# Kernel optimization log

Measured on AMD Instinct MI355X. Metric: run time of the kernel, lower is better.

## Reference

```python
import jax, jax.numpy as jnp
import numpy as np

H = 2048          # hidden_size
NH = 16           # num_attention_heads
HD = H // NH      # head_dim = 128
SCALE = 1.0 / np.sqrt(HD)


def setup_inputs() -> dict:
    key = jax.random.key(0)
    k1, k2, k3 = jax.random.split(key, 3)
    hidden_states = jax.random.normal(k1, (4, 2048, H), dtype=jnp.float32)
    # Linear weights stored as [in, out] (torch stores [out, in]; math y = x @ W + b)
    W_attn = jax.random.normal(k2, (H, 3 * H), dtype=jnp.float32) * 0.02
    b_attn = jnp.zeros((3 * H,), dtype=jnp.float32)
    W_proj = jax.random.normal(k3, (H, H), dtype=jnp.float32) * 0.02
    b_proj = jnp.zeros((H,), dtype=jnp.float32)
    return {"hidden_states": hidden_states, "W_attn": W_attn, "b_attn": b_attn,
            "W_proj": W_proj, "b_proj": b_proj}


def reference(hidden_states, W_attn, b_attn, W_proj, b_proj):
    B, S, _ = hidden_states.shape
    qkv = hidden_states @ W_attn + b_attn            # [B, S, 3H]
    q, k, v = jnp.split(qkv, 3, axis=-1)
    # split heads -> [B, NH, S, HD]
    def split_heads(t):
        return t.reshape(B, S, NH, HD).transpose(0, 2, 1, 3)
    q, k, v = split_heads(q), split_heads(k), split_heads(v)
    scores = jnp.einsum('bhqd,bhkd->bhqk', q, k) * SCALE   # [B, NH, S, S]
    causal = jnp.tril(jnp.ones((S, S), dtype=bool))
    scores = jnp.where(causal, scores, jnp.finfo(scores.dtype).min)
    attn = jax.nn.softmax(scores, axis=-1)
    out = jnp.einsum('bhqk,bhkd->bhqd', attn, v)           # [B, NH, S, HD]
    out = out.transpose(0, 2, 1, 3).reshape(B, S, H)       # merge heads
    out = out @ W_proj + b_proj
    return out
```

## Files before the change

kernel.cpp:

```cpp
#include <hip/hip_runtime.h>
#include <hip/hip_bf16.h>

typedef __bf16 bf16x8 __attribute__((ext_vector_type(8)));
typedef float  f32x4  __attribute__((ext_vector_type(4)));
typedef __hip_bfloat16 bf16;

#define MFMA16(a,b,c) __builtin_amdgcn_mfma_f32_16x16x32_bf16(a,b,c,0,0,0)

__device__ __forceinline__ void gload_lds16(const void* g, void* l){
  __builtin_amdgcn_global_load_lds((const __attribute__((address_space(1))) void*)g,
                                   (__attribute__((address_space(3))) void*)l, 16, 0, 0);
}

__global__ __launch_bounds__(256) void k_cvt(const float* __restrict__ in,
                                             bf16* __restrict__ out, int n4){
  int stride = gridDim.x * blockDim.x;
  for (int i = blockIdx.x * blockDim.x + threadIdx.x; i < n4; i += stride){
    float4 v = ((const float4*)in)[i];
    bf16 o[4] = {__float2bfloat16(v.x), __float2bfloat16(v.y),
                 __float2bfloat16(v.z), __float2bfloat16(v.w)};
    *(ushort4*)(out + 4*(size_t)i) = *(ushort4*)o;
  }
}

__global__ __launch_bounds__(256) void k_tr(const float* __restrict__ in,
                                            bf16* __restrict__ out, int R, int C){
  __shared__ float t[32][33];
  int c0 = blockIdx.x*32, r0 = blockIdx.y*32;
  int x = threadIdx.x, y0 = threadIdx.y;
  for (int j = y0; j < 32; j += 8) t[j][x] = in[(size_t)(r0+j)*C + c0 + x];
  __syncthreads();
  for (int j = y0; j < 32; j += 8)
    out[(size_t)(c0+j)*R + r0 + x] = __float2bfloat16(t[x][j]);
}

template<bool OUTF32>
__global__ __launch_bounds__(256,2) void k_gemm(const bf16* __restrict__ A,
                                                const bf16* __restrict__ Bt,
                                                const float* __restrict__ bias,
                                                void* __restrict__ Cv,
                                                int M, int N, int K){
  __shared__ bf16 As[128*32];
  __shared__ bf16 Bs[128*32];
  const int tid = threadIdx.x, w = tid>>6, l = tid&63;
  const int wm = w>>1, wn = w&1, lg = l>>4, li = l&15;
  const int m0 = blockIdx.y*128, n0 = blockIdx.x*128;

  f32x4 acc[4][4];
  #pragma unroll
  for (int m=0;m<4;m++)
    #pragma unroll
    for (int n=0;n<4;n++) acc[m][n] = (f32x4){0.f,0.f,0.f,0.f};

  for (int k0 = 0; k0 < K; k0 += 32){
    #pragma unroll
    for (int i=0;i<2;i++){
      int u = i*256 + w*64 + l;
      int r = u>>2, c = (u&3)*8;
      gload_lds16(A  + (size_t)(m0+r)*K + k0 + c, As + (size_t)(i*256 + w*64)*8);
      gload_lds16(Bt + (size_t)(n0+r)*K + k0 + c, Bs + (size_t)(i*256 + w*64)*8);
    }
    __syncthreads();
    bf16x8 af[4], bfv[4];
    #pragma unroll
    for (int m=0;m<4;m++) af[m]  = *(const bf16x8*)(As + (size_t)(wm*64 + m*16 + li)*32 + lg*8);
    #pragma unroll
    for (int n=0;n<4;n++) bfv[n] = *(const bf16x8*)(Bs + (size_t)(wn*64 + n*16 + li)*32 + lg*8);
    #pragma unroll
    for (int m=0;m<4;m++)
      #pragma unroll
      for (int n=0;n<4;n++)
        acc[m][n] = MFMA16(af[m], bfv[n], acc[m][n]);
    __syncthreads();
  }

  #pragma unroll
  for (int m=0;m<4;m++)
    #pragma unroll
    for (int n=0;n<4;n++)
      #pragma unroll
      for (int r4=0;r4<4;r4++){
        int row = m0 + wm*64 + m*16 + lg*4 + r4;
        int col = n0 + wn*64 + n*16 + li;
        float v = acc[m][n][r4] + bias[col];
        if (OUTF32) ((float*)Cv)[(size_t)row*N + col] = v;
        else        ((bf16*)Cv)[(size_t)row*N + col] = __float2bfloat16(v);
      }
}

#define ATT_SCALE 0.08838834764831845f

__global__ __launch_bounds__(256,2) void k_attn(const bf16* __restrict__ qkv,
                                                bf16* __restrict__ O){
  const int qb = blockIdx.x, h = blockIdx.y, b = blockIdx.z;
  const int tid = threadIdx.x, w = tid>>6, l = tid&63;
  const int lg = l>>4, li = l&15;
  const size_t RS = 6144;

  __shared__ bf16 Kt[64][136];
  __shared__ bf16 Vt[128][72];
  __shared__ bf16 Pt[4][32][72];

  const bf16* qptr = qkv + ((size_t)(b*2048 + qb*128 + w*32))*RS + h*128;
  bf16x8 qf[2][4];
  #pragma unroll
  for (int m=0;m<2;m++)
    #pragma unroll
    for (int ks=0;ks<4;ks++)
      qf[m][ks] = *(const bf16x8*)(qptr + (size_t)(m*16+li)*RS + ks*32 + lg*8);

  f32x4 acc[2][8];
  #pragma unroll
  for (int m=0;m<2;m++)
    #pragma unroll
    for (int n=0;n<8;n++) acc[m][n] = (f32x4){0.f,0.f,0.f,0.f};
  float mst[8], lst[8];
  #pragma unroll
  for (int i=0;i<8;i++){ mst[i] = -1e30f; lst[i] = 0.f; }

  const int nkt = 2*(qb+1);
  for (int kt = 0; kt < nkt; ++kt){
    const bf16* kbase = qkv + ((size_t)(b*2048 + kt*64))*RS + 2048 + h*128;
    #pragma unroll
    for (int i=0;i<4;i++){
      int u = i*256 + tid;
      int r = u>>4, c = (u&15)*8;
      *(bf16x8*)(&Kt[r][c]) = *(const bf16x8*)(kbase + (size_t)r*RS + c);
    }
    const bf16* vbase = qkv + ((size_t)(b*2048 + kt*64))*RS + 4096 + h*128;
    #pragma unroll
    for (int i=0;i<4;i++){
      int key = i*16 + (tid&15);
      int d0  = ((tid>>4)&15)*8;
      bf16x8 v = *(const bf16x8*)(vbase + (size_t)key*RS + d0);
      #pragma unroll
      for (int j=0;j<8;j++) Vt[d0+j][key] = ((const bf16*)&v)[j];
    }
    __syncthreads();

    f32x4 s[2][4];
    #pragma unroll
    for (int m=0;m<2;m++)
      #pragma unroll
      for (int n=0;n<4;n++) s[m][n] = (f32x4){0.f,0.f,0.f,0.f};
    #pragma unroll
    for (int ks=0;ks<4;ks++){
      bf16x8 kf[4];
      #pragma unroll
      for (int n=0;n<4;n++) kf[n] = *(const bf16x8*)(&Kt[n*16+li][ks*32 + lg*8]);
      #pragma unroll
      for (int m=0;m<2;m++)
        #pragma unroll
        for (int n=0;n<4;n++) s[m][n] = MFMA16(qf[m][ks], kf[n], s[m][n]);
    }

    #pragma unroll
    for (int m=0;m<2;m++)
      #pragma unroll
      for (int n=0;n<4;n++){
        int key = kt*64 + n*16 + li;
        #pragma unroll
        for (int r4=0;r4<4;r4++){
          int qrow = qb*128 + w*32 + m*16 + lg*4 + r4;
          float v = s[m][n][r4]*ATT_SCALE;
          s[m][n][r4] = (key <= qrow) ? v : -1e30f;
        }
      }

    #pragma unroll
    for (int m=0;m<2;m++)
      #pragma unroll
      for (int r4=0;r4<4;r4++){
        int idx = m*4 + r4;
        float rm = fmaxf(fmaxf(s[m][0][r4], s[m][1][r4]),
                         fmaxf(s[m][2][r4], s[m][3][r4]));
        rm = fmaxf(rm, __shfl_xor(rm, 1));
        rm = fmaxf(rm, __shfl_xor(rm, 2));
        rm = fmaxf(rm, __shfl_xor(rm, 4));
        rm = fmaxf(rm, __shfl_xor(rm, 8));
        float mnew = fmaxf(mst[idx], rm);
        float corr = __expf(mst[idx] - mnew);
        mst[idx] = mnew;
        float ps = 0.f;
        #pragma unroll
        for (int n=0;n<4;n++){
          float p = __expf(s[m][n][r4] - mnew);
          s[m][n][r4] = p; ps += p;
        }
        ps += __shfl_xor(ps, 1);
        ps += __shfl_xor(ps, 2);
        ps += __shfl_xor(ps, 4);
        ps += __shfl_xor(ps, 8);
        lst[idx] = lst[idx]*corr + ps;
        #pragma unroll
        for (int n=0;n<8;n++) acc[m][n][r4] *= corr;
      }

    #pragma unroll
    for (int m=0;m<2;m++)
      #pragma unroll
      for (int n=0;n<4;n++)
        #pragma unroll
        for (int r4=0;r4<4;r4++)
          Pt[w][m*16 + lg*4 + r4][n*16 + li] = __float2bfloat16(s[m][n][r4]);

    #pragma unroll
    for (int ks=0;ks<2;ks++){
      bf16x8 pa[2];
      #pragma unroll
      for (int m=0;m<2;m++) pa[m] = *(const bf16x8*)(&Pt[w][m*16+li][ks*32 + lg*8]);
      #pragma unroll
      for (int n=0;n<8;n++){
        bf16x8 vf = *(const bf16x8*)(&Vt[n*16+li][ks*32 + lg*8]);
        #pragma unroll
        for (int m=0;m<2;m++) acc[m][n] = MFMA16(pa[m], vf, acc[m][n]);
      }
    }
    __syncthreads();
  }

  bf16* obase = O + ((size_t)(b*2048 + qb*128 + w*32))*2048 + h*128;
  #pragma unroll
  for (int m=0;m<2;m++)
    #pragma unroll
    for (int n=0;n<8;n++)
      #pragma unroll
      for (int r4=0;r4<4;r4++){
        float v = acc[m][n][r4] / lst[m*4 + r4];
        obase[(size_t)(m*16 + lg*4 + r4)*2048 + n*16 + li] = __float2bfloat16(v);
      }
}

extern "C" void kernel_launch(void* const* d_in, const int* in_sizes, int n_in,
                              void* d_out, int out_size, void* d_ws, size_t ws_size,
                              hipStream_t stream) {
  const float* X      = (const float*)d_in[0];
  const float* W_attn = (const float*)d_in[1];
  const float* b_attn = (const float*)d_in[2];
  const float* W_proj = (const float*)d_in[3];
  const float* b_proj = (const float*)d_in[4];
  float* out = (float*)d_out;

  char* ws = (char*)d_ws;
  bf16* Xb  = (bf16*)(ws);
  bf16* Wat = (bf16*)(ws + 33554432);
  bf16* Wpt = (bf16*)(ws + 58720256);
  bf16* QKV = (bf16*)(ws + 67108864);
  bf16* Obf = Xb;

  k_cvt<<<2048, 256, 0, stream>>>(X, Xb, 8192*2048/4);
  k_tr <<<dim3(192,64), dim3(32,8), 0, stream>>>(W_attn, Wat, 2048, 6144);
  k_tr <<<dim3(64,64),  dim3(32,8), 0, stream>>>(W_proj, Wpt, 2048, 2048);

  k_gemm<false><<<dim3(48,64), 256, 0, stream>>>(Xb, Wat, b_attn, (void*)QKV, 8192, 6144, 2048);

  k_attn<<<dim3(16,16,4), 256, 0, stream>>>(QKV, Obf);

  k_gemm<true><<<dim3(16,64), 256, 0, stream>>>(Obf, Wpt, b_proj, (void*)out, 8192, 2048, 2048);
}
```

Baseline: 649.7 us.

## Swizzle attention LDS tiles, load K via direct-to-LDS, and reverse query block order

Replaces the padded LDS arrays for K, V and P in the attention kernel with unpadded byte buffers that use an XOR swizzle on 16-byte chunks to avoid bank conflicts. K tiles are now loaded with global_load_lds, which writes straight into LDS and skips the register round trip, and the global source address is permuted to match the swizzle. Query blocks are also launched in reverse so the longest causal blocks start first, which should improve load balance across the grid. The added risk is that the swizzle index math has to agree exactly between the global_load_lds writes, which are placed per wave and lane, and the reads.

```diff
diff --git a/kernel.cpp b/kernel.cpp
--- a/kernel.cpp
+++ b/kernel.cpp
@@ -11,6 +11,8 @@
   __builtin_amdgcn_global_load_lds((const __attribute__((address_space(1))) void*)g,
                                    (__attribute__((address_space(3))) void*)l, 16, 0, 0);
 }
+
+__device__ __forceinline__ int swzb(int row){ return ((row ^ (row>>3)) & 7) << 4; }
 
 __global__ __launch_bounds__(256) void k_cvt(const float* __restrict__ in,
                                              bf16* __restrict__ out, int n4){
@@ -92,14 +94,15 @@
 
 __global__ __launch_bounds__(256,2) void k_attn(const bf16* __restrict__ qkv,
                                                 bf16* __restrict__ O){
-  const int qb = blockIdx.x, h = blockIdx.y, b = blockIdx.z;
+  const int qb = 15 - blockIdx.x, h = blockIdx.y, b = blockIdx.z;
   const int tid = threadIdx.x, w = tid>>6, l = tid&63;
   const int lg = l>>4, li = l&15;
   const size_t RS = 6144;
-
-  __shared__ bf16 Kt[64][136];
-  __shared__ bf16 Vt[128][72];
-  __shared__ bf16 Pt[4][32][72];
+  const size_t RSB = RS*2;
+
+  __shared__ char Kt[64*256];
+  __shared__ char Vt[128*128];
+  __shared__ char Pt[4][32*128];
 
   const bf16* qptr = qkv + ((size_t)(b*2048 + qb*128 + w*32))*RS + h*128;
   bf16x8 qf[2][4];
@@ -120,12 +123,13 @@
 
   const int nkt = 2*(qb+1);
   for (int kt = 0; kt < nkt; ++kt){
-    const bf16* kbase = qkv + ((size_t)(b*2048 + kt*64))*RS + 2048 + h*128;
+    const char* kbase = (const char*)(qkv + ((size_t)(b*2048 + kt*64))*RS + 2048 + h*128);
     #pragma unroll
     for (int i=0;i<4;i++){
       int u = i*256 + tid;
-      int r = u>>4, c = (u&15)*8;
-      *(bf16x8*)(&Kt[r][c]) = *(const bf16x8*)(kbase + (size_t)r*RS + c);
+      int r = u>>4, cbl = (u&15)*16;
+      int cg = cbl ^ swzb(r);
+      gload_lds16(kbase + (size_t)r*RSB + cg, Kt + i*4096 + w*1024);
     }
     const bf16* vbase = qkv + ((size_t)(b*2048 + kt*64))*RS + 4096 + h*128;
     #pragma unroll
@@ -134,7 +138,8 @@
       int d0  = ((tid>>4)&15)*8;
       bf16x8 v = *(const bf16x8*)(vbase + (size_t)key*RS + d0);
       #pragma unroll
-      for (int j=0;j<8;j++) Vt[d0+j][key] = ((const bf16*)&v)[j];
+      for (int j=0;j<8;j++)
+        *(bf16*)(Vt + (d0+j)*128 + ((key*2) ^ swzb(d0+j))) = ((const bf16*)&v)[j];
     }
     __syncthreads();
 
@@ -147,7 +152,10 @@
     for (int ks=0;ks<4;ks++){
       bf16x8 kf[4];
       #pragma unroll
-      for (int n=0;n<4;n++) kf[n] = *(const bf16x8*)(&Kt[n*16+li][ks*32 + lg*8]);
+      for (int n=0;n<4;n++){
+        int row = n*16+li;
+        kf[n] = *(const bf16x8*)(Kt + row*256 + ((ks*64+lg*16) ^ swzb(row)));
+      }
       #pragma unroll
       for (int m=0;m<2;m++)
         #pragma unroll
@@ -201,17 +209,24 @@
       #pragma unroll
       for (int n=0;n<4;n++)
         #pragma unroll
-        for (int r4=0;r4<4;r4++)
-          Pt[w][m*16 + lg*4 + r4][n*16 + li] = __float2bfloat16(s[m][n][r4]);
+        for (int r4=0;r4<4;r4++){
+          int row = m*16 + lg*4 + r4;
+          *(bf16*)(Pt[w] + row*128 + (((n*16+li)*2) ^ swzb(row))) =
+              __float2bfloat16(s[m][n][r4]);
+        }
 
     #pragma unroll
     for (int ks=0;ks<2;ks++){
       bf16x8 pa[2];
       #pragma unroll
-      for (int m=0;m<2;m++) pa[m] = *(const bf16x8*)(&Pt[w][m*16+li][ks*32 + lg*8]);
+      for (int m=0;m<2;m++){
+        int row = m*16+li;
+        pa[m] = *(const bf16x8*)(Pt[w] + row*128 + ((ks*64+lg*16) ^ swzb(row)));
+      }
       #pragma unroll
       for (int n=0;n<8;n++){
-        bf16x8 vf = *(const bf16x8*)(&Vt[n*16+li][ks*32 + lg*8]);
+        int row = n*16+li;
+        bf16x8 vf = *(const bf16x8*)(Vt + row*128 + ((ks*64+lg*16) ^ swzb(row)));
         #pragma unroll
         for (int m=0;m<2;m++) acc[m][n] = MFMA16(pa[m], vf, acc[m][n]);
       }
```

Result: slower. 1.071 ms (+64.8%).
